# Kernel optimization log

Measured on AMD Instinct MI355X. Metric: run time of the kernel, lower is better.

## Reference

```python
import jax, jax.numpy as jnp
import numpy as np

N = 10000           # nodes
E = 160000          # edges
MUL = 128           # multiplicity of each irrep (128x0e + 128x1o)
EDGE_FEAT = 8       # radial embedding dim
AVG_NUM_NEIGHBORS = 16.0
MLP_IN = MUL + MUL + EDGE_FEAT + 1  # 265
NUM_W = 4 * MUL     # irreps_mid num_irreps = 256x0e + 256x1o -> 512 path weights
SQ3 = float(np.sqrt(3.0))


def setup_inputs() -> dict:
    key = jax.random.key(0)
    ks = jax.random.split(key, 16)
    node_feats = jax.random.normal(ks[0], (N, 4 * MUL), dtype=jnp.float32)  # [N,512] = 128x0e ++ 128x1o
    edge_attrs = jax.random.normal(ks[1], (E, 4), dtype=jnp.float32)        # 1x0e ++ 1x1o
    edge_feats = jax.random.normal(ks[2], (E, EDGE_FEAT), dtype=jnp.float32)
    lengths = jax.random.uniform(ks[3], (E, 1), dtype=jnp.float32)
    edge_index = jax.random.randint(ks[4], (2, E), 0, N, dtype=jnp.int32)
    # e3nn Linear weights (stored unit-variance; forward applies 1/sqrt(fan_in))
    W_scalar = jax.random.normal(ks[5], (MUL, MUL), dtype=jnp.float32)
    W_up0 = jax.random.normal(ks[6], (MUL, MUL), dtype=jnp.float32)
    W_up1 = jax.random.normal(ks[7], (MUL, MUL), dtype=jnp.float32)
    # conv_tp_weights MLP (flax Dense: fan-scaled init, bias on first two layers)
    W1 = jax.random.normal(ks[8], (MLP_IN, MUL), dtype=jnp.float32) / np.sqrt(MLP_IN)
    b1 = jnp.zeros((MUL,), dtype=jnp.float32)
    W2 = jax.random.normal(ks[9], (MUL, MUL), dtype=jnp.float32) / np.sqrt(MUL)
    b2 = jnp.zeros((MUL,), dtype=jnp.float32)
    W3 = jax.random.normal(ks[10], (MUL, NUM_W), dtype=jnp.float32) / np.sqrt(MUL)
    # final e3nn Linear: 256x0e+256x1o -> 128x0e+128x1o
    Wout0 = jax.random.normal(ks[11], (2 * MUL, MUL), dtype=jnp.float32)
    Wout1 = jax.random.normal(ks[12], (2 * MUL, MUL), dtype=jnp.float32)
    return {"node_feats": node_feats, "edge_attrs": edge_attrs, "edge_feats": edge_feats,
            "lengths": lengths, "edge_index": edge_index, "W_scalar": W_scalar,
            "W_up0": W_up0, "W_up1": W_up1, "W1": W1, "b1": b1, "W2": W2, "b2": b2,
            "W3": W3, "Wout0": Wout0, "Wout1": Wout1}


def reference(node_feats, edge_attrs, edge_feats, lengths, edge_index,
              W_scalar, W_up0, W_up1, W1, b1, W2, b2, W3, Wout0, Wout1):
    n = node_feats.shape[0]
    inv = 1.0 / np.sqrt(MUL)
    x0 = node_feats[:, :MUL]                       # [N,128]   0e
    x1 = node_feats[:, MUL:].reshape(n, MUL, 3)    # [N,128,3] 1o

    # linear_scalar: only 0e->0e path survives
    scalars = (x0 @ W_scalar) * inv                # [N,128]
    # linear_up: per-irrep channel mixing
    h0 = (x0 @ W_up0) * inv                        # [N,128]
    h1 = jnp.einsum('nmi,mo->noi', x1, W_up1) * inv  # [N,128,3]

    sender, receiver = edge_index[0], edge_index[1]

    # conv_tp_weights MLP
    mlp_in = jnp.concatenate([scalars[sender], scalars[receiver], edge_feats, lengths], axis=-1)
    h = jax.nn.silu(mlp_in @ W1 + b1)
    h = jax.nn.silu(h @ W2 + b2)
    tpw = h @ W3                                   # [E,512]

    xs0 = h0[sender]                               # [E,128]
    xs1 = h1[sender]                               # [E,128,3]
    y0 = edge_attrs[:, 0:1]                        # [E,1]  0e
    y1 = edge_attrs[:, 1:4]                        # [E,3]  1o

    # CG tensor product (component normalization), filtered to {0e,1o}; sorted order:
    # 0e block = [0e*0e->0e, 1o*1o->0e], 1o block = [0e*1o->1o, 1o*0e->1o]
    mA = xs0 * y0                                       # [E,128]   0e
    mD = (xs1 * y1[:, None, :]).sum(-1) / SQ3           # [E,128]   0e
    mB = xs0[:, :, None] * y1[:, None, :]               # [E,128,3] 1o
    mC = xs1 * y0[:, :, None]                           # [E,128,3] 1o

    # per-irrep path weights (one scalar per irrep channel)
    wA, wD = tpw[:, :MUL], tpw[:, MUL:2 * MUL]
    wB, wC = tpw[:, 2 * MUL:3 * MUL], tpw[:, 3 * MUL:]

    m0 = jnp.concatenate([mA * wA, mD * wD], axis=1)                          # [E,256]
    m1 = jnp.concatenate([mB * wB[:, :, None], mC * wC[:, :, None]], axis=1)  # [E,256,3]

    # scatter-sum aggregation to receivers
    agg0 = jax.ops.segment_sum(m0, receiver, num_segments=n)  # [N,256]
    agg1 = jax.ops.segment_sum(m1, receiver, num_segments=n)  # [N,256,3]

    # final e3nn Linear + / avg_num_neighbors
    scale = 1.0 / (np.sqrt(2 * MUL) * AVG_NUM_NEIGHBORS)
    out0 = (agg0 @ Wout0) * scale                             # [N,128]
    out1 = jnp.einsum('nmi,mo->noi', agg1, Wout1) * scale     # [N,128,3]

    # reshape_irreps: [N, mul, sum(ir dims)] = [N,128,4]
    return jnp.concatenate([out0[:, :, None], out1], axis=-1)
```

## Files before the change

kernel.cpp:

```cpp
#include <hip/hip_runtime.h>
#include <hip/hip_bf16.h>

#define NN 10000
#define NE 160000
#define TILE 32
#define A1S 296
#define A2S 136

typedef __attribute__((ext_vector_type(8))) short short8;
typedef __attribute__((ext_vector_type(4))) float f32x4;

__device__ __forceinline__ float silu_f(float x) { return x / (1.0f + __expf(-x)); }
__device__ __forceinline__ unsigned short bf16u(float v) {
    __hip_bfloat16 b = __float2bfloat16(v);
    return *reinterpret_cast<unsigned short*>(&b);
}
__device__ __forceinline__ short8 pack8(float4 a, float4 b) {
    short8 r;
    r[0]=(short)bf16u(a.x); r[1]=(short)bf16u(a.y); r[2]=(short)bf16u(a.z); r[3]=(short)bf16u(a.w);
    r[4]=(short)bf16u(b.x); r[5]=(short)bf16u(b.y); r[6]=(short)bf16u(b.z); r[7]=(short)bf16u(b.w);
    return r;
}

#define OFF_W1  0
#define OFF_W2  36864
#define OFF_W3  53248
#define OFF_WSC 118784
#define OFF_WU0 135168
#define OFF_WU1 151552
#define OFF_WO0 167936
#define OFF_WO1 200704
#define WP_TOTAL 233472

__global__ __launch_bounds__(256) void convert_weights(
    const float* __restrict__ W1, const float* __restrict__ W2,
    const float* __restrict__ W3, const float* __restrict__ Wsc,
    const float* __restrict__ Wu0, const float* __restrict__ Wu1,
    const float* __restrict__ Wo0, const float* __restrict__ Wo1,
    unsigned short* __restrict__ wp)
{
    int idx = blockIdx.x * 256 + threadIdx.x;
    if (idx >= WP_TOTAL) return;
    const float* src; int off, N, K;
    if      (idx < OFF_W2)  { src = W1;  off = OFF_W1;  N = 128; K = 265; }
    else if (idx < OFF_W3)  { src = W2;  off = OFF_W2;  N = 128; K = 128; }
    else if (idx < OFF_WSC) { src = W3;  off = OFF_W3;  N = 512; K = 128; }
    else if (idx < OFF_WU0) { src = Wsc; off = OFF_WSC; N = 128; K = 128; }
    else if (idx < OFF_WU1) { src = Wu0; off = OFF_WU0; N = 128; K = 128; }
    else if (idx < OFF_WO0) { src = Wu1; off = OFF_WU1; N = 128; K = 128; }
    else if (idx < OFF_WO1) { src = Wo0; off = OFF_WO0; N = 128; K = 256; }
    else                    { src = Wo1; off = OFF_WO1; N = 128; K = 256; }
    int j = idx - off;
    int kt = j / (N * 32);
    int rem = j % (N * 32);
    int n = rem >> 5, kk = rem & 31;
    int k = kt * 32 + kk;
    wp[idx] = (k < K) ? bf16u(src[k * N + n]) : (unsigned short)0;
}

__global__ __launch_bounds__(256) void node_transform(
    const float* __restrict__ node_feats,
    const unsigned short* __restrict__ wp,
    unsigned short* __restrict__ scalars_bf,
    float* __restrict__ h0,
    float* __restrict__ h1t)
{
    __shared__ unsigned short xls[4 * 16 * 136];
    const int t = threadIdx.x;
    const int bn = blockIdx.x * 16;

    for (int i = t; i < 16 * 512; i += 256) {
        int n = i >> 9, j = i & 511;
        unsigned short u = bf16u(node_feats[(size_t)(bn + n) * 512 + j]);
        if (j < 128) xls[n * 136 + j] = u;
        else {
            int jj = j - 128;
            int m = jj / 3;
            int c = jj - 3 * m;
            xls[(1 + c) * 2176 + n * 136 + m] = u;
        }
    }
    __syncthreads();

    const int wv = t >> 6, lane = t & 63, l16 = lane & 15, l4 = lane >> 4;
    const unsigned short* Wscp = wp + OFF_WSC;
    const unsigned short* Wu0p = wp + OFF_WU0;
    const unsigned short* Wu1p = wp + OFF_WU1;

    f32x4 asc[2] = {}, ah0[2] = {}, ah1[3][2] = {};
    for (int kt = 0; kt < 4; ++kt) {
        short8 ax0 = *(const short8*)(xls + l16 * 136 + kt * 32 + l4 * 8);
        short8 ax1[3];
        #pragma unroll
        for (int c = 0; c < 3; ++c)
            ax1[c] = *(const short8*)(xls + (1 + c) * 2176 + l16 * 136 + kt * 32 + l4 * 8);
        #pragma unroll
        for (int n = 0; n < 2; ++n) {
            int col = wv * 32 + n * 16 + l16;
            short8 bsc = *(const short8*)(Wscp + ((size_t)kt * 128 + col) * 32 + l4 * 8);
            short8 bu0 = *(const short8*)(Wu0p + ((size_t)kt * 128 + col) * 32 + l4 * 8);
            short8 bu1 = *(const short8*)(Wu1p + ((size_t)kt * 128 + col) * 32 + l4 * 8);
            asc[n] = __builtin_amdgcn_mfma_f32_16x16x32_bf16(ax0, bsc, asc[n], 0, 0, 0);
            ah0[n] = __builtin_amdgcn_mfma_f32_16x16x32_bf16(ax0, bu0, ah0[n], 0, 0, 0);
            #pragma unroll
            for (int c = 0; c < 3; ++c)
                ah1[c][n] = __builtin_amdgcn_mfma_f32_16x16x32_bf16(ax1[c], bu1, ah1[c][n], 0, 0, 0);
        }
    }
    const float inv = 0.08838834764831845f;
    #pragma unroll
    for (int n = 0; n < 2; ++n) {
        int col = wv * 32 + n * 16 + l16;
        #pragma unroll
        for (int r = 0; r < 4; ++r) {
            int node = bn + l4 * 4 + r;
            scalars_bf[(size_t)node * 128 + col] = bf16u(asc[n][r] * inv);
            h0[(size_t)node * 128 + col] = ah0[n][r] * inv;
            #pragma unroll
            for (int c = 0; c < 3; ++c)
                h1t[(size_t)c * NN * 128 + (size_t)node * 128 + col] = ah1[c][n][r] * inv;
        }
    }
}

__global__ __launch_bounds__(256) void hist_kernel(const int* __restrict__ edge_index,
                                                   int* __restrict__ deg) {
    int e = blockIdx.x * 256 + threadIdx.x;
    if (e < NE) atomicAdd(&deg[edge_index[NE + e]], 1);
}

__global__ __launch_bounds__(256) void scan_kernel(const int* __restrict__ deg,
                                                   int* __restrict__ cursor) {
    __shared__ int s[256];
    const int t = threadIdx.x;
    const int base = t * 40;
    int ld[40];
    int lsum = 0;
    #pragma unroll
    for (int i = 0; i < 40; ++i) {
        int idx = base + i;
        ld[i] = (idx < NN) ? deg[idx] : 0;
        lsum += ld[i];
    }
    s[t] = lsum;
    __syncthreads();
    for (int off = 1; off < 256; off <<= 1) {
        int u = (t >= off) ? s[t - off] : 0;
        __syncthreads();
        s[t] += u;
        __syncthreads();
    }
    int run = s[t] - lsum;
    #pragma unroll
    for (int i = 0; i < 40; ++i) {
        int idx = base + i;
        if (idx < NN) cursor[idx] = run;
        run += ld[i];
    }
}

__global__ __launch_bounds__(256) void perm_kernel(const int* __restrict__ edge_index,
                                                   int* __restrict__ cursor,
                                                   int* __restrict__ perm) {
    int e = blockIdx.x * 256 + threadIdx.x;
    if (e < NE) {
        int r = edge_index[NE + e];
        int pos = atomicAdd(&cursor[r], 1);
        perm[pos] = e;
    }
}

__global__ __launch_bounds__(256, 5) void edge_kernel(
    const unsigned short* __restrict__ scalars_bf,
    const float* __restrict__ h0g,
    const float* __restrict__ h1t,
    const float* __restrict__ edge_attrs,
    const float* __restrict__ edge_feats,
    const float* __restrict__ lengths,
    const int* __restrict__ edge_index,
    const int* __restrict__ perm,
    const float* __restrict__ b1, const float* __restrict__ b2,
    const unsigned short* __restrict__ wp,
    float* __restrict__ agg0, float* __restrict__ agg1t)
{
    __shared__ unsigned char smem_u[27648];
    __shared__ int   eid_s[TILE];
    __shared__ int   s_s[TILE];
    __shared__ int   r_s[TILE];
    __shared__ float4 y_s[TILE];

    unsigned short* A1 = (unsigned short*)smem_u;
    unsigned short* A2 = (unsigned short*)(smem_u + 18944);
    unsigned short* A3 = A1;
    float* PKh = (float*)(smem_u + 8704);

    const int t = threadIdx.x;
    const int e0 = blockIdx.x * TILE;
    const int wv = t >> 6;
    const int lane = t & 63;
    const int l16 = lane & 15;
    const int l4 = lane >> 4;

    if (t < TILE) {
        int eid = perm[e0 + t];
        eid_s[t] = eid;
        s_s[t] = edge_index[eid];
        r_s[t] = edge_index[NE + eid];
        y_s[t] = *(const float4*)(edge_attrs + (size_t)eid * 4);
    }
    __syncthreads();

    {
        const int e = t >> 3, j = t & 7;
        const unsigned short* srow = scalars_bf + (size_t)s_s[e] * 128;
        const unsigned short* rrow = scalars_bf + (size_t)r_s[e] * 128;
        *(uint4*)(A1 + e*A1S + j*16)       = *(const uint4*)(srow + j*16);
        *(uint4*)(A1 + e*A1S + j*16 + 8)   = *(const uint4*)(srow + j*16 + 8);
        *(uint4*)(A1 + e*A1S + 128 + j*16)     = *(const uint4*)(rrow + j*16);
        *(uint4*)(A1 + e*A1S + 128 + j*16 + 8) = *(const uint4*)(rrow + j*16 + 8);
        A1[e*A1S + 256 + j] = bf16u(edge_feats[(size_t)eid_s[e] * 8 + j]);
        if (t < TILE) A1[t*A1S + 264] = bf16u(lengths[eid_s[t]]);
        for (int i = t; i < TILE * 23; i += 256) {
            int row = i / 23, c = 265 + (i - row * 23);
            A1[row*A1S + c] = 0;
        }
    }
    __syncthreads();

    const unsigned short* Wp1 = wp + OFF_W1;
    const unsigned short* Wp2 = wp + OFF_W2;
    const unsigned short* Wp3 = wp + OFF_W3;

    {
        f32x4 acc[2][2] = {};
        for (int kt = 0; kt < 9; ++kt) {
            short8 a0 = *(const short8*)(A1 + (     l16)*A1S + kt*32 + l4*8);
            short8 a1 = *(const short8*)(A1 + (16 + l16)*A1S + kt*32 + l4*8);
            #pragma unroll
            for (int n = 0; n < 2; ++n) {
                int col = (2*wv + n)*16 + l16;
                short8 b = *(const short8*)(Wp1 + ((size_t)kt*128 + col)*32 + l4*8);
                acc[0][n] = __builtin_amdgcn_mfma_f32_16x16x32_bf16(a0, b, acc[0][n], 0, 0, 0);
                acc[1][n] = __builtin_amdgcn_mfma_f32_16x16x32_bf16(a1, b, acc[1][n], 0, 0, 0);
            }
        }
        #pragma unroll
        for (int n = 0; n < 2; ++n) {
            int col = (2*wv + n)*16 + l16;
            float bb = b1[col];
            #pragma unroll
            for (int m = 0; m < 2; ++m)
                #pragma unroll
                for (int r = 0; r < 4; ++r) {
                    int row = m*16 + l4*4 + r;
                    A2[row*A2S + col] = bf16u(silu_f(acc[m][n][r] + bb));
                }
        }
    }
    __syncthreads();

    {
        f32x4 acc[2][2] = {};
        for (int kt = 0; kt < 4; ++kt) {
            short8 a0 = *(const short8*)(A2 + (     l16)*A2S + kt*32 + l4*8);
            short8 a1 = *(const short8*)(A2 + (16 + l16)*A2S + kt*32 + l4*8);
            #pragma unroll
            for (int n = 0; n < 2; ++n) {
                int col = (2*wv + n)*16 + l16;
                short8 b = *(const short8*)(Wp2 + ((size_t)kt*128 + col)*32 + l4*8);
                acc[0][n] = __builtin_amdgcn_mfma_f32_16x16x32_bf16(a0, b, acc[0][n], 0, 0, 0);
                acc[1][n] = __builtin_amdgcn_mfma_f32_16x16x32_bf16(a1, b, acc[1][n], 0, 0, 0);
            }
        }
        #pragma unroll
        for (int n = 0; n < 2; ++n) {
            int col = (2*wv + n)*16 + l16;
            float bb = b2[col];
            #pragma unroll
            for (int m = 0; m < 2; ++m)
                #pragma unroll
                for (int r = 0; r < 4; ++r) {
                    int row = m*16 + l4*4 + r;
                    A3[row*A2S + col] = bf16u(silu_f(acc[m][n][r] + bb));
                }
        }
    }
    __syncthreads();

    const float rs3 = 0.57735026918962576f;
    #pragma unroll
    for (int pass = 0; pass < 2; ++pass) {
        const int base0 = pass ? 128 : 0;
        const int base1 = pass ? 384 : 256;
        for (int hh = 0; hh < 2; ++hh) {
            f32x4 acc[2][2] = {};
            for (int kt = 0; kt < 4; ++kt) {
                short8 a0 = *(const short8*)(A3 + (     l16)*A2S + kt*32 + l4*8);
                short8 a1 = *(const short8*)(A3 + (16 + l16)*A2S + kt*32 + l4*8);
                #pragma unroll
                for (int fam = 0; fam < 2; ++fam) {
                    int col = (fam ? base1 : base0) + hh*64 + wv*16 + l16;
                    short8 b = *(const short8*)(Wp3 + ((size_t)kt*512 + col)*32 + l4*8);
                    acc[fam][0] = __builtin_amdgcn_mfma_f32_16x16x32_bf16(a0, b, acc[fam][0], 0, 0, 0);
                    acc[fam][1] = __builtin_amdgcn_mfma_f32_16x16x32_bf16(a1, b, acc[fam][1], 0, 0, 0);
                }
            }
            #pragma unroll
            for (int fam = 0; fam < 2; ++fam)
                #pragma unroll
                for (int m = 0; m < 2; ++m)
                    #pragma unroll
                    for (int r = 0; r < 4; ++r) {
                        int row = m*16 + l4*4 + r;
                        float y0 = y_s[row].x;
                        float fold = (fam == 0) ? (pass ? rs3 : y0) : (pass ? y0 : 1.0f);
                        PKh[row*132 + fam*64 + wv*16 + l16] = acc[fam][m][r] * fold;
                    }
            __syncthreads();

            {
                const int q = t >> 6, o = t & 63;
                const int ocol = hh*64 + o;
                const int rlo = q * 8;
                float ac0 = 0.f, ac1 = 0.f, ac2 = 0.f, ac3 = 0.f;
                int run_start = rlo;
                int prev_rn = r_s[rlo];

                auto flush = [&](int rn, bool interior) {
                    size_t b0 = (size_t)rn * 256 + base0 + ocol;
                    if (interior) {
                        agg0[b0] = ac0;
                        agg1t[0*(size_t)NN*256 + b0] = ac1;
                        agg1t[1*(size_t)NN*256 + b0] = ac2;
                        agg1t[2*(size_t)NN*256 + b0] = ac3;
                    } else {
                        atomicAdd(agg0 + b0, ac0);
                        atomicAdd(agg1t + 0*(size_t)NN*256 + b0, ac1);
                        atomicAdd(agg1t + 1*(size_t)NN*256 + b0, ac2);
                        atomicAdd(agg1t + 2*(size_t)NN*256 + b0, ac3);
                    }
                };

                for (int row = rlo; row < rlo + 8; ++row) {
                    int rn = r_s[row];
                    if (rn != prev_rn) {
                        flush(prev_rn, run_start > rlo);
                        ac0 = ac1 = ac2 = ac3 = 0.f;
                        run_start = row;
                        prev_rn = rn;
                    }
                    int sn = s_s[row];
                    float w0 = PKh[row*132 + o];
                    float w1 = PKh[row*132 + 64 + o];
                    float4 y = y_s[row];
                    if (pass == 0) {
                        float x = h0g[(size_t)sn*128 + ocol];
                        ac0 = fmaf(x, w0, ac0);
                        float xb = x * w1;
                        ac1 = fmaf(xb, y.y, ac1);
                        ac2 = fmaf(xb, y.z, ac2);
                        ac3 = fmaf(xb, y.w, ac3);
                    } else {
                        float xx = h1t[0*NN*128 + (size_t)sn*128 + ocol];
                        float xy = h1t[1*NN*128 + (size_t)sn*128 + ocol];
                        float xz = h1t[2*NN*128 + (size_t)sn*128 + ocol];
                        float dd = xx*y.y + xy*y.z + xz*y.w;
                        ac0 = fmaf(dd, w0, ac0);
                        ac1 = fmaf(xx, w1, ac1);
                        ac2 = fmaf(xy, w1, ac2);
                        ac3 = fmaf(xz, w1, ac3);
                    }
                }
                flush(prev_rn, false);
            }
            __syncthreads();
        }
    }
}

__global__ __launch_bounds__(256) void output_transform(
    const float* __restrict__ agg0,
    const float* __restrict__ agg1t,
    const unsigned short* __restrict__ wp,
    float* __restrict__ out)
{
    __shared__ unsigned short As[4][16 * 264];
    const int t = threadIdx.x;
    const int bn = blockIdx.x * 16;

    for (int i = t; i < 2048; i += 256) {
        int mat = i >> 9;
        int rem = i & 511;
        int n = rem >> 5;
        int ko = (rem & 31) * 8;
        const float* src = (mat == 0)
            ? (agg0 + (size_t)(bn + n) * 256 + ko)
            : (agg1t + (size_t)(mat - 1) * NN * 256 + (size_t)(bn + n) * 256 + ko);
        float4 v0 = *(const float4*)(src);
        float4 v1 = *(const float4*)(src + 4);
        *(short8*)(&As[mat][n * 264 + ko]) = pack8(v0, v1);
    }
    __syncthreads();

    const int wv = t >> 6, lane = t & 63, l16 = lane & 15, l4 = lane >> 4;
    const unsigned short* Wo0p = wp + OFF_WO0;
    const unsigned short* Wo1p = wp + OFF_WO1;

    f32x4 acc[2][4] = {};
    for (int kt = 0; kt < 8; ++kt) {
        short8 a0 = *(const short8*)(&As[0][l16 * 264 + kt * 32 + l4 * 8]);
        short8 a1 = *(const short8*)(&As[1][l16 * 264 + kt * 32 + l4 * 8]);
        short8 a2 = *(const short8*)(&As[2][l16 * 264 + kt * 32 + l4 * 8]);
        short8 a3 = *(const short8*)(&As[3][l16 * 264 + kt * 32 + l4 * 8]);
        #pragma unroll
        for (int n = 0; n < 2; ++n) {
            int col = wv * 32 + n * 16 + l16;
            short8 bw0 = *(const short8*)(Wo0p + ((size_t)kt * 128 + col) * 32 + l4 * 8);
            short8 bw1 = *(const short8*)(Wo1p + ((size_t)kt * 128 + col) * 32 + l4 * 8);
            acc[n][0] = __builtin_amdgcn_mfma_f32_16x16x32_bf16(a0, bw0, acc[n][0], 0, 0, 0);
            acc[n][1] = __builtin_amdgcn_mfma_f32_16x16x32_bf16(a1, bw1, acc[n][1], 0, 0, 0);
            acc[n][2] = __builtin_amdgcn_mfma_f32_16x16x32_bf16(a2, bw1, acc[n][2], 0, 0, 0);
            acc[n][3] = __builtin_amdgcn_mfma_f32_16x16x32_bf16(a3, bw1, acc[n][3], 0, 0, 0);
        }
    }
    const float scale = 0.00390625f;
    #pragma unroll
    for (int n = 0; n < 2; ++n) {
        int col = wv * 32 + n * 16 + l16;
        #pragma unroll
        for (int r = 0; r < 4; ++r) {
            int node = bn + l4 * 4 + r;
            float4 v = make_float4(acc[n][0][r] * scale, acc[n][1][r] * scale,
                                   acc[n][2][r] * scale, acc[n][3][r] * scale);
            *(float4*)(out + ((size_t)node * 128 + col) * 4) = v;
        }
    }
}

extern "C" void kernel_launch(void* const* d_in, const int* in_sizes, int n_in,
                              void* d_out, int out_size, void* d_ws, size_t ws_size,
                              hipStream_t stream) {
    const float* node_feats = (const float*)d_in[0];
    const float* edge_attrs = (const float*)d_in[1];
    const float* edge_feats = (const float*)d_in[2];
    const float* lengths    = (const float*)d_in[3];
    const int*   edge_index = (const int*)d_in[4];
    const float* W_scalar   = (const float*)d_in[5];
    const float* W_up0      = (const float*)d_in[6];
    const float* W_up1      = (const float*)d_in[7];
    const float* W1         = (const float*)d_in[8];
    const float* b1         = (const float*)d_in[9];
    const float* W2         = (const float*)d_in[10];
    const float* b2         = (const float*)d_in[11];
    const float* W3         = (const float*)d_in[12];
    const float* Wout0      = (const float*)d_in[13];
    const float* Wout1      = (const float*)d_in[14];

    float* ws = (float*)d_ws;
    unsigned short* scalars_bf = (unsigned short*)ws;
    float* h0    = ws + 640000;
    float* h1t   = ws + 1920000;
    float* agg0  = ws + 5760000;
    float* agg1t = ws + 8320000;
    unsigned short* wpack = (unsigned short*)(ws + 16000000);
    int* deg    = (int*)(ws + 16116736);
    int* cursor = (int*)(ws + 16126736);
    int* perm   = (int*)(ws + 16136736);
    if (ws_size < 16296736ull * 4ull) return;

    hipMemsetAsync(agg0, 0, 10240000ull * 4ull, stream);
    hipMemsetAsync(deg, 0, NN * 4, stream);
    convert_weights<<<(WP_TOTAL + 255) / 256, 256, 0, stream>>>(
        W1, W2, W3, W_scalar, W_up0, W_up1, Wout0, Wout1, wpack);
    node_transform<<<625, 256, 0, stream>>>(node_feats, wpack, scalars_bf, h0, h1t);
    hist_kernel<<<(NE + 255) / 256, 256, 0, stream>>>(edge_index, deg);
    scan_kernel<<<1, 256, 0, stream>>>(deg, cursor);
    perm_kernel<<<(NE + 255) / 256, 256, 0, stream>>>(edge_index, cursor, perm);
    edge_kernel<<<NE / TILE, 256, 0, stream>>>(scalars_bf, h0, h1t, edge_attrs, edge_feats, lengths,
                                               edge_index, perm, b1, b2, wpack, agg0, agg1t);
    output_transform<<<625, 256, 0, stream>>>(agg0, agg1t, wpack, (float*)d_out);
}
```

Baseline: 240.1 us.

## Prefetch sender node features into registers early; widen scan; merge memsets

```diff
diff --git a/kernel.cpp b/kernel.cpp
--- a/kernel.cpp
+++ b/kernel.cpp
@@ -129,22 +129,22 @@
     if (e < NE) atomicAdd(&deg[edge_index[NE + e]], 1);
 }
 
-__global__ __launch_bounds__(256) void scan_kernel(const int* __restrict__ deg,
-                                                   int* __restrict__ cursor) {
-    __shared__ int s[256];
+__global__ __launch_bounds__(1024) void scan_kernel(const int* __restrict__ deg,
+                                                    int* __restrict__ cursor) {
+    __shared__ int s[1024];
     const int t = threadIdx.x;
-    const int base = t * 40;
-    int ld[40];
+    const int base = t * 10;
+    int ld[10];
     int lsum = 0;
     #pragma unroll
-    for (int i = 0; i < 40; ++i) {
+    for (int i = 0; i < 10; ++i) {
         int idx = base + i;
         ld[i] = (idx < NN) ? deg[idx] : 0;
         lsum += ld[i];
     }
     s[t] = lsum;
     __syncthreads();
-    for (int off = 1; off < 256; off <<= 1) {
+    for (int off = 1; off < 1024; off <<= 1) {
         int u = (t >= off) ? s[t - off] : 0;
         __syncthreads();
         s[t] += u;
@@ -152,7 +152,7 @@
     }
     int run = s[t] - lsum;
     #pragma unroll
-    for (int i = 0; i < 40; ++i) {
+    for (int i = 0; i < 10; ++i) {
         int idx = base + i;
         if (idx < NN) cursor[idx] = run;
         run += ld[i];
@@ -170,7 +170,7 @@
     }
 }
 
-__global__ __launch_bounds__(256, 5) void edge_kernel(
+__global__ __launch_bounds__(256, 4) void edge_kernel(
     const unsigned short* __restrict__ scalars_bf,
     const float* __restrict__ h0g,
     const float* __restrict__ h1t,
@@ -225,6 +225,24 @@
             A1[row*A1S + c] = 0;
         }
     }
+
+    const int q = t >> 6, o = t & 63;
+    const int rlo = q * 8;
+    float pf0[16];
+    float pf1[48];
+    #pragma unroll
+    for (int i = 0; i < 8; ++i) {
+        int sn = s_s[rlo + i];
+        const float* h0r = h0g + (size_t)sn * 128 + o;
+        pf0[i]     = h0r[0];
+        pf0[8 + i] = h0r[64];
+        #pragma unroll
+        for (int c = 0; c < 3; ++c) {
+            const float* h1r = h1t + (size_t)c * NN * 128 + (size_t)sn * 128 + o;
+            pf1[c*16 + i]     = h1r[0];
+            pf1[c*16 + 8 + i] = h1r[64];
+        }
+    }
     __syncthreads();
 
     const unsigned short* Wp1 = wp + OFF_W1;
@@ -292,6 +310,7 @@
     for (int pass = 0; pass < 2; ++pass) {
         const int base0 = pass ? 128 : 0;
         const int base1 = pass ? 384 : 256;
+        #pragma unroll
         for (int hh = 0; hh < 2; ++hh) {
             f32x4 acc[2][2] = {};
             for (int kt = 0; kt < 4; ++kt) {
@@ -319,9 +338,7 @@
             __syncthreads();
 
             {
-                const int q = t >> 6, o = t & 63;
                 const int ocol = hh*64 + o;
-                const int rlo = q * 8;
                 float ac0 = 0.f, ac1 = 0.f, ac2 = 0.f, ac3 = 0.f;
                 int run_start = rlo;
                 int prev_rn = r_s[rlo];
@@ -341,7 +358,9 @@
                     }
                 };
 
-                for (int row = rlo; row < rlo + 8; ++row) {
+                #pragma unroll
+                for (int i = 0; i < 8; ++i) {
+                    int row = rlo + i;
                     int rn = r_s[row];
                     if (rn != prev_rn) {
                         flush(prev_rn, run_start > rlo);
@@ -349,21 +368,20 @@
                         run_start = row;
                         prev_rn = rn;
                     }
-                    int sn = s_s[row];
                     float w0 = PKh[row*132 + o];
                     float w1 = PKh[row*132 + 64 + o];
                     float4 y = y_s[row];
                     if (pass == 0) {
-                        float x = h0g[(size_t)sn*128 + ocol];
+                        float x = pf0[hh*8 + i];
                         ac0 = fmaf(x, w0, ac0);
                         float xb = x * w1;
                         ac1 = fmaf(xb, y.y, ac1);
                         ac2 = fmaf(xb, y.z, ac2);
                         ac3 = fmaf(xb, y.w, ac3);
                     } else {
-                        float xx = h1t[0*NN*128 + (size_t)sn*128 + ocol];
-                        float xy = h1t[1*NN*128 + (size_t)sn*128 + ocol];
-                        float xz = h1t[2*NN*128 + (size_t)sn*128 + ocol];
+                        float xx = pf1[0*16 + hh*8 + i];
+                        float xy = pf1[1*16 + hh*8 + i];
+                        float xz = pf1[2*16 + hh*8 + i];
                         float dd = xx*y.y + xy*y.z + xz*y.w;
                         ac0 = fmaf(dd, w0, ac0);
                         ac1 = fmaf(xx, w1, ac1);
@@ -462,19 +480,18 @@
     float* h1t   = ws + 1920000;
     float* agg0  = ws + 5760000;
     float* agg1t = ws + 8320000;
-    unsigned short* wpack = (unsigned short*)(ws + 16000000);
-    int* deg    = (int*)(ws + 16116736);
-    int* cursor = (int*)(ws + 16126736);
-    int* perm   = (int*)(ws + 16136736);
+    int* deg    = (int*)(ws + 16000000);
+    int* cursor = (int*)(ws + 16010000);
+    int* perm   = (int*)(ws + 16020000);
+    unsigned short* wpack = (unsigned short*)(ws + 16180000);
     if (ws_size < 16296736ull * 4ull) return;
 
-    hipMemsetAsync(agg0, 0, 10240000ull * 4ull, stream);
-    hipMemsetAsync(deg, 0, NN * 4, stream);
+    hipMemsetAsync(agg0, 0, 10250000ull * 4ull, stream);
     convert_weights<<<(WP_TOTAL + 255) / 256, 256, 0, stream>>>(
         W1, W2, W3, W_scalar, W_up0, W_up1, Wout0, Wout1, wpack);
     node_transform<<<625, 256, 0, stream>>>(node_feats, wpack, scalars_bf, h0, h1t);
     hist_kernel<<<(NE + 255) / 256, 256, 0, stream>>>(edge_index, deg);
-    scan_kernel<<<1, 256, 0, stream>>>(deg, cursor);
+    scan_kernel<<<1, 1024, 0, stream>>>(deg, cursor);
     perm_kernel<<<(NE + 255) / 256, 256, 0, stream>>>(edge_index, cursor, perm);
     edge_kernel<<<NE / TILE, 256, 0, stream>>>(scalars_bf, h0, h1t, edge_attrs, edge_feats, lengths,
                                                edge_index, perm, b1, b2, wpack, agg0, agg1t);
```

After: 261.4 us. 1.09x slower.
